# Performance work log

Hardware: AMD Instinct MI355X
Metric: run time of the kernel (lower is better)

Reference implementation:

```python
import jax, jax.numpy as jnp
import numpy as np

DIM = 64
HEADS = 4
EPS_LN = 1e-6
EPS_NORM = 1e-12


def _dwconv(x, w):
    # depthwise 3x3, SAME padding; x: [B,C,H,W], w: [C,1,3,3]
    return jax.lax.conv_general_dilated(
        x, w, window_strides=(1, 1), padding='SAME',
        feature_group_count=x.shape[1],
        dimension_numbers=('NCHW', 'OIHW', 'NCHW'))


def setup_inputs() -> dict:
    key = jax.random.key(0)
    ks = jax.random.split(key, 10)
    s = 0.05
    inp = {
        'x': jax.random.normal(ks[0], (8, DIM, 256, 256), dtype=jnp.float32),
        'ln_w': jnp.ones((DIM,), jnp.float32),
        'ln_b': jnp.zeros((DIM,), jnp.float32),
        'w_q': jax.random.normal(ks[1], (DIM, DIM), jnp.float32) * s,
        'w_k': jax.random.normal(ks[2], (DIM, DIM), jnp.float32) * s,
        'w_v': jax.random.normal(ks[3], (DIM, DIM), jnp.float32) * s,
        'dw_q': jax.random.normal(ks[4], (DIM, 1, 3, 3), jnp.float32) * s,
        'dw_k': jax.random.normal(ks[5], (DIM, 1, 3, 3), jnp.float32) * s,
        'dw_v': jax.random.normal(ks[6], (DIM, 1, 3, 3), jnp.float32) * s,
        'w_proj': jax.random.normal(ks[7], (DIM, DIM, 3, 3), jnp.float32) * s,
        'w_comp': jax.random.normal(ks[8], (DIM // 4, DIM), jnp.float32) * s,
        'temperature': jnp.ones((HEADS, 1, 1), jnp.float32),
    }
    return inp


def reference(x, ln_w, ln_b, w_q, w_k, w_v, dw_q, dw_k, dw_v, w_proj, w_comp, temperature):
    b, c, h, w = x.shape
    heads = temperature.shape[0]
    hd = c // heads  # per-head channels

    # LayerNorm over channel dim (per spatial location), biased variance
    mu = jnp.mean(x, axis=1, keepdims=True)
    var = jnp.mean((x - mu) ** 2, axis=1, keepdims=True)
    xn = (x - mu) / jnp.sqrt(var + EPS_LN)
    xn = xn * ln_w[None, :, None, None] + ln_b[None, :, None, None]

    # 1x1 projections then depthwise 3x3
    q = _dwconv(jnp.einsum('oc,bchw->bohw', w_q, xn), dw_q)
    k = _dwconv(jnp.einsum('oc,bchw->bohw', w_k, xn), dw_k)
    v = _dwconv(jnp.einsum('oc,bchw->bohw', w_v, xn), dw_v)

    # [b, heads, hd, h*w]
    q = q.reshape(b, heads, hd, h * w)
    k = k.reshape(b, heads, hd, h * w)
    v = v.reshape(b, heads, hd, h * w)

    # L2 normalize along spatial axis (torch F.normalize: x / max(||x||, eps))
    q = q / jnp.maximum(jnp.linalg.norm(q, axis=-1, keepdims=True), EPS_NORM)
    k = k / jnp.maximum(jnp.linalg.norm(k, axis=-1, keepdims=True), EPS_NORM)

    # channel attention: [b, heads, hd, hd]
    attn = jnp.einsum('bhcn,bhdn->bhcd', q, k) * temperature[None]
    attn = jax.nn.softmax(attn, axis=-1)
    out = jnp.einsum('bhcd,bhdn->bhcn', attn, v).reshape(b, c, h, w)

    # 3x3 projection + residual (residual is the normalized x, per source)
    out = jax.lax.conv_general_dilated(
        out, w_proj, window_strides=(1, 1), padding='SAME',
        dimension_numbers=('NCHW', 'OIHW', 'NCHW')) + xn

    # 1x1 compress to dim//4
    return jnp.einsum('oc,bchw->bohw', w_comp, out)
```

## Files before the change

### kernel.cpp

```cpp
#include <hip/hip_runtime.h>
#include <hip/hip_bf16.h>
#include <stdint.h>

#define BB 8
#define CC 64
#define HH 256
#define WW 256
#define NPIX 65536
#define HEADS 4
#define HD 16
#define PRS 76

using bf16 = __hip_bfloat16;
typedef __attribute__((ext_vector_type(8))) short short8;
typedef __attribute__((ext_vector_type(4))) float f32x4;

__device__ __forceinline__ float bf2f(bf16 v) { return __bfloat162float(v); }
__device__ __forceinline__ bf16 f2bf(float v) { return __float2bfloat16(v); }
__device__ __forceinline__ short f2bfs(float f) { bf16 h = __float2bfloat16(f); return *reinterpret_cast<short*>(&h); }
__device__ __forceinline__ float bfs2f(short s) { return __uint_as_float(((uint32_t)(uint16_t)s) << 16); }
__device__ __forceinline__ uint32_t pk2(float a, float b) {
  return (uint32_t)(uint16_t)f2bfs(a) | ((uint32_t)(uint16_t)f2bfs(b) << 16);
}
__device__ __forceinline__ short8 zero8() { short8 z = {0, 0, 0, 0, 0, 0, 0, 0}; return z; }

__global__ void k_prep(const float* __restrict__ w_comp, const float* __restrict__ w_proj,
                       const float* __restrict__ w_q, const float* __restrict__ w_k,
                       const float* __restrict__ w_v,
                       short* __restrict__ wcpb, short* __restrict__ wqkvb,
                       short* __restrict__ wcb) {
  int idx = blockIdx.x * 256 + threadIdx.x;
  if (idx < 9 * 16 * 64) {
    int c = idx & 63;
    int o = (idx >> 6) & 15;
    int kk = idx >> 10;
    float acc = 0.f;
    for (int m = 0; m < 64; ++m)
      acc += w_comp[o * 64 + m] * w_proj[(m * 64 + c) * 9 + kk];
    wcpb[idx] = f2bfs(acc);
  }
  if (idx < 3 * 4096) {
    const float* Ws[3] = {w_q, w_k, w_v};
    wqkvb[idx] = f2bfs(Ws[idx >> 12][idx & 4095]);
  }
  if (idx < 1024) wcb[idx] = f2bfs(w_comp[idx]);
}

__global__ __launch_bounds__(256)
void k_ln(const float* __restrict__ x, const float* __restrict__ ln_w,
          const float* __restrict__ ln_b, short* __restrict__ xnb) {
  const int tid = threadIdx.x;
  const int b = blockIdx.x >> 8;
  const int n = ((blockIdx.x & 255) << 8) + tid;
  const float* xp = x + (size_t)b * CC * NPIX + n;
  float v[64];
  float s = 0.f, s2 = 0.f;
#pragma unroll
  for (int c = 0; c < 64; ++c) {
    float t0 = xp[(size_t)c * NPIX];
    v[c] = t0; s += t0; s2 += t0 * t0;
  }
  const float mu = s * (1.f / 64.f);
  const float r = rsqrtf(s2 * (1.f / 64.f) - mu * mu + 1e-6f);
  short* op = xnb + ((size_t)b * NPIX + n) * 64;
#pragma unroll
  for (int c8 = 0; c8 < 8; ++c8) {
    uint32_t pk[4];
#pragma unroll
    for (int j = 0; j < 4; ++j) {
      const int c0 = c8 * 8 + 2 * j;
      float f0 = (v[c0] - mu) * r * ln_w[c0] + ln_b[c0];
      float f1 = (v[c0 + 1] - mu) * r * ln_w[c0 + 1] + ln_b[c0 + 1];
      pk[j] = pk2(f0, f1);
    }
    *reinterpret_cast<uint4*>(op + c8 * 8) = make_uint4(pk[0], pk[1], pk[2], pk[3]);
  }
}

__global__ __launch_bounds__(512)
void k_qkv(const short* __restrict__ xnb, const short* __restrict__ wqkvb,
           const short* __restrict__ wcb,
           const float* __restrict__ dw_q, const float* __restrict__ dw_k,
           const float* __restrict__ dw_v,
           bf16* __restrict__ qo, bf16* __restrict__ ko,
           short* __restrict__ aov, short* __restrict__ res16) {
  __shared__ short pr_s[336 * PRS];
  const int tid = threadIdx.x;
  const int lane = tid & 63;
  const int wv = tid >> 6;
  const int olocal = lane & 15;
  const int g = lane >> 4;
  const int t = blockIdx.y;
  const int tx = blockIdx.x & 15, ty = (blockIdx.x >> 4) & 15, b = blockIdx.x >> 8;
  const int x0 = tx * 16 - 1, y0 = ty * 16 - 1;

  if (t == 0) {
    short8 wc0 = *reinterpret_cast<const short8*>(wcb + olocal * 64 + g * 8);
    short8 wc1 = *reinterpret_cast<const short8*>(wcb + olocal * 64 + 32 + g * 8);
#pragma unroll
    for (int t2 = 0; t2 < 2; ++t2) {
      const int oy = wv * 2 + t2;
      const int n = (ty * 16 + oy) * WW + tx * 16 + olocal;
      const short* bb = xnb + ((size_t)b * NPIX + n) * 64 + g * 8;
      short8 b0 = *reinterpret_cast<const short8*>(bb);
      short8 b1 = *reinterpret_cast<const short8*>(bb + 32);
      f32x4 acc = {0.f, 0.f, 0.f, 0.f};
      acc = __builtin_amdgcn_mfma_f32_16x16x32_bf16(wc0, b0, acc, 0, 0, 0);
      acc = __builtin_amdgcn_mfma_f32_16x16x32_bf16(wc1, b1, acc, 0, 0, 0);
      uint2 st;
      st.x = pk2(acc[0], acc[1]);
      st.y = pk2(acc[2], acc[3]);
      *reinterpret_cast<uint2*>(&res16[((size_t)b * NPIX + n) * 16 + g * 4]) = st;
    }
  }

  short8 Bt[4][2];
#pragma unroll
  for (int ot = 0; ot < 4; ++ot) {
    const short* wb = wqkvb + t * 4096 + (ot * 16 + olocal) * 64 + g * 8;
    Bt[ot][0] = *reinterpret_cast<const short8*>(wb);
    Bt[ot][1] = *reinterpret_cast<const short8*>(wb + 32);
  }

  short8 a0[3], a1[3];
#pragma unroll
  for (int j = 0; j < 3; ++j) {
    const int pt = wv + j * 8;
    const int p = pt * 16 + olocal;
    const int py = y0 + p / 18;
    const int px_ = x0 + p % 18;
    const bool vld = (pt < 21) && (p < 324) && ((unsigned)py < 256u) && ((unsigned)px_ < 256u);
    if (vld) {
      const short* ab = xnb + ((size_t)b * NPIX + py * WW + px_) * 64 + g * 8;
      a0[j] = *reinterpret_cast<const short8*>(ab);
      a1[j] = *reinterpret_cast<const short8*>(ab + 32);
    } else {
      a0[j] = zero8();
      a1[j] = zero8();
    }
  }
#pragma unroll
  for (int j = 0; j < 3; ++j) {
    const int pt = wv + j * 8;
    if (pt >= 21) continue;
    const int p2 = pt * 16 + olocal;
#pragma unroll
    for (int ot = 0; ot < 4; ++ot) {
      f32x4 acc = {0.f, 0.f, 0.f, 0.f};
      acc = __builtin_amdgcn_mfma_f32_16x16x32_bf16(Bt[ot][0], a0[j], acc, 0, 0, 0);
      acc = __builtin_amdgcn_mfma_f32_16x16x32_bf16(Bt[ot][1], a1[j], acc, 0, 0, 0);
      uint2 st;
      st.x = pk2(acc[0], acc[1]);
      st.y = pk2(acc[2], acc[3]);
      *reinterpret_cast<uint2*>(&pr_s[p2 * PRS + ot * 16 + g * 4]) = st;
    }
  }
  __syncthreads();

  const float* dmt = (t == 0) ? dw_q : (t == 1) ? dw_k : dw_v;
  float dmr[8][9];
#pragma unroll
  for (int u = 0; u < 8; ++u)
#pragma unroll
    for (int kk = 0; kk < 9; ++kk)
      dmr[u][kk] = dmt[(wv * 8 + u) * 9 + kk];
  bf16* ob = ((t == 0) ? qo : ko) + (size_t)b * CC * NPIX;
#pragma unroll
  for (int i = 0; i < 4; ++i) {
    const int pxl = lane + i * 64;
    const int oy = pxl >> 4, ox = pxl & 15;
    float acc8[8] = {0.f, 0.f, 0.f, 0.f, 0.f, 0.f, 0.f, 0.f};
#pragma unroll
    for (int ky = 0; ky < 3; ++ky)
#pragma unroll
      for (int kx = 0; kx < 3; ++kx) {
        const short8 pv = *reinterpret_cast<const short8*>(
            &pr_s[((oy + ky) * 18 + ox + kx) * PRS + wv * 8]);
        const int kk = ky * 3 + kx;
#pragma unroll
        for (int u = 0; u < 8; ++u)
          acc8[u] += dmr[u][kk] * bfs2f(pv[u]);
      }
    const int n = (ty * 16 + oy) * WW + tx * 16 + ox;
    if (t < 2) {
#pragma unroll
      for (int u = 0; u < 8; ++u)
        ob[(size_t)(wv * 8 + u) * NPIX + n] = f2bf(acc8[u]);
    } else {
      uint4 st = make_uint4(pk2(acc8[0], acc8[1]), pk2(acc8[2], acc8[3]),
                            pk2(acc8[4], acc8[5]), pk2(acc8[6], acc8[7]));
      *reinterpret_cast<uint4*>(&aov[((size_t)b * NPIX + n) * 64 + wv * 8]) = st;
    }
  }
}

__global__ __launch_bounds__(256)
void k_logits(const bf16* __restrict__ q, const bf16* __restrict__ kk_,
              float* __restrict__ Spart, float* __restrict__ Qpart,
              float* __restrict__ Kpart) {
  const int tid = threadIdx.x;
  const int lane = tid & 63;
  const int wv = tid >> 6;
  const int bh = blockIdx.x >> 5;
  const int chunk = blockIdx.x & 31;
  const int row = lane & 15;
  const int g = lane >> 4;
  const short* qp = (const short*)q + (size_t)(bh * HD + row) * NPIX;
  const short* kp = (const short*)kk_ + (size_t)(bh * HD + row) * NPIX;
  const int n0 = chunk * 2048 + wv * 512 + g * 8;
  f32x4 s = {0.f, 0.f, 0.f, 0.f};
  f32x4 sq = {0.f, 0.f, 0.f, 0.f};
  f32x4 sk = {0.f, 0.f, 0.f, 0.f};
#pragma unroll
  for (int it = 0; it < 16; ++it) {
    const int n = n0 + it * 32;
    short8 qa = *reinterpret_cast<const short8*>(qp + n);
    short8 ka = *reinterpret_cast<const short8*>(kp + n);
    s  = __builtin_amdgcn_mfma_f32_16x16x32_bf16(qa, ka, s, 0, 0, 0);
    sq = __builtin_amdgcn_mfma_f32_16x16x32_bf16(qa, qa, sq, 0, 0, 0);
    sk = __builtin_amdgcn_mfma_f32_16x16x32_bf16(ka, ka, sk, 0, 0, 0);
  }
  const size_t tile = (size_t)blockIdx.x * 4 + wv;
  float* sp = Spart + tile * 256;
#pragma unroll
  for (int r = 0; r < 4; ++r)
    sp[(g * 4 + r) * 16 + row] = s[r];
  if ((row >> 2) == g) {
    Qpart[tile * 16 + row] = sq[row & 3];
    Kpart[tile * 16 + row] = sk[row & 3];
  }
}

__global__ __launch_bounds__(256)
void k_softmax(const float* __restrict__ Spart, const float* __restrict__ Qpart,
               const float* __restrict__ Kpart, const float* __restrict__ temp,
               short* __restrict__ attb) {
  const int tid = threadIdx.x;
  const int bh = blockIdx.x;
  const int b = bh >> 2, h = bh & 3;
  const int i = tid >> 4, j = tid & 15;
  float S = 0.f, qs = 0.f, ks = 0.f;
  const size_t t0 = (size_t)bh * 128;
  for (int c = 0; c < 128; ++c) {
    S += Spart[(t0 + c) * 256 + tid];
    qs += Qpart[(t0 + c) * 16 + i];
    ks += Kpart[(t0 + c) * 16 + j];
  }
  float nq = fmaxf(sqrtf(qs), 1e-12f);
  float nk = fmaxf(sqrtf(ks), 1e-12f);
  float val = S / (nq * nk) * temp[h];
  float m = val;
  for (int d = 1; d < 16; d <<= 1) m = fmaxf(m, __shfl_xor(m, d));
  float e = __expf(val - m);
  float s = e;
  for (int d = 1; d < 16; d <<= 1) s += __shfl_xor(s, d);
  attb[((size_t)b * 64 + h * 16 + i) * 64 + h * 16 + j] = f2bfs(e / s);
#pragma unroll
  for (int mq = 0; mq < 4; ++mq) {
    const int idx = tid * 4 + mq;
    const int r = idx >> 6, c = idx & 63;
    if ((c >> 4) != h)
      attb[((size_t)b * 64 + h * 16 + r) * 64 + c] = 0;
  }
}

__global__ __launch_bounds__(512)
void k_attf(const short* __restrict__ attb, const short* __restrict__ vao,
            const short* __restrict__ wcpb, const short* __restrict__ res16,
            float* __restrict__ out) {
  __shared__ short ao_s[336 * PRS];
  const int tid = threadIdx.x;
  const int lane = tid & 63;
  const int wv = tid >> 6;
  const int olocal = lane & 15;
  const int g = lane >> 4;
  const int tx = blockIdx.x & 15, ty = (blockIdx.x >> 4) & 15, b = blockIdx.x >> 8;
  const int x0 = tx * 16 - 1, y0 = ty * 16 - 1;

  {
    short8 AT[4][2];
#pragma unroll
    for (int ot = 0; ot < 4; ++ot) {
      const short* ab = attb + ((size_t)b * 64 + ot * 16 + olocal) * 64 + g * 8;
      AT[ot][0] = *reinterpret_cast<const short8*>(ab);
      AT[ot][1] = *reinterpret_cast<const short8*>(ab + 32);
    }
#pragma unroll
    for (int j = 0; j < 3; ++j) {
      const int pt = wv + j * 8;
      if (pt >= 21) continue;
      const int p = pt * 16 + olocal;
      const int py = y0 + p / 18;
      const int px_ = x0 + p % 18;
      const bool vld = (p < 324) && ((unsigned)py < 256u) && ((unsigned)px_ < 256u);
      short8 b0 = zero8(), b1 = zero8();
      if (vld) {
        const short* vp = vao + ((size_t)b * NPIX + py * WW + px_) * 64 + g * 8;
        b0 = *reinterpret_cast<const short8*>(vp);
        b1 = *reinterpret_cast<const short8*>(vp + 32);
      }
#pragma unroll
      for (int ot = 0; ot < 4; ++ot) {
        f32x4 acc = {0.f, 0.f, 0.f, 0.f};
        acc = __builtin_amdgcn_mfma_f32_16x16x32_bf16(AT[ot][0], b0, acc, 0, 0, 0);
        acc = __builtin_amdgcn_mfma_f32_16x16x32_bf16(AT[ot][1], b1, acc, 0, 0, 0);
        uint2 st;
        st.x = pk2(acc[0], acc[1]);
        st.y = pk2(acc[2], acc[3]);
        *reinterpret_cast<uint2*>(&ao_s[p * PRS + ot * 16 + g * 4]) = st;
      }
    }
  }
  __syncthreads();

  short8 WA[9][2];
#pragma unroll
  for (int kk = 0; kk < 9; ++kk) {
    const short* wb = wcpb + (kk * 16 + olocal) * 64 + g * 8;
    WA[kk][0] = *reinterpret_cast<const short8*>(wb);
    WA[kk][1] = *reinterpret_cast<const short8*>(wb + 32);
  }
#pragma unroll
  for (int s = 0; s < 2; ++s) {
    const int oy = wv * 2 + s;
    const int n0 = (ty * 16 + oy) * WW + tx * 16;
    uint2 rv = *reinterpret_cast<const uint2*>(
        &res16[((size_t)b * NPIX + n0 + olocal) * 16 + g * 4]);
    f32x4 acc;
    acc[0] = __uint_as_float(rv.x << 16);
    acc[1] = __uint_as_float(rv.x & 0xffff0000u);
    acc[2] = __uint_as_float(rv.y << 16);
    acc[3] = __uint_as_float(rv.y & 0xffff0000u);
#pragma unroll
    for (int ky = 0; ky < 3; ++ky)
#pragma unroll
      for (int kx = 0; kx < 3; ++kx) {
        const int hp = (oy + ky) * 18 + olocal + kx;
        short8 b0 = *reinterpret_cast<const short8*>(&ao_s[hp * PRS + g * 8]);
        short8 b1 = *reinterpret_cast<const short8*>(&ao_s[hp * PRS + 32 + g * 8]);
        acc = __builtin_amdgcn_mfma_f32_16x16x32_bf16(WA[ky * 3 + kx][0], b0, acc, 0, 0, 0);
        acc = __builtin_amdgcn_mfma_f32_16x16x32_bf16(WA[ky * 3 + kx][1], b1, acc, 0, 0, 0);
      }
    float* op = out + ((size_t)b * 16 + g * 4) * NPIX + n0 + olocal;
    op[0] = acc[0];
    op[NPIX] = acc[1];
    op[2 * NPIX] = acc[2];
    op[3 * NPIX] = acc[3];
  }
}

extern "C" void kernel_launch(void* const* d_in, const int* in_sizes, int n_in,
                              void* d_out, int out_size, void* d_ws, size_t ws_size,
                              hipStream_t stream) {
  const float* x      = (const float*)d_in[0];
  const float* ln_w   = (const float*)d_in[1];
  const float* ln_b   = (const float*)d_in[2];
  const float* w_q    = (const float*)d_in[3];
  const float* w_k    = (const float*)d_in[4];
  const float* w_v    = (const float*)d_in[5];
  const float* dw_q   = (const float*)d_in[6];
  const float* dw_k   = (const float*)d_in[7];
  const float* dw_v   = (const float*)d_in[8];
  const float* w_proj = (const float*)d_in[9];
  const float* w_comp = (const float*)d_in[10];
  const float* temp   = (const float*)d_in[11];
  float* out = (float*)d_out;

  const size_t SPX = (size_t)BB * NPIX;
  short* xnb   = (short*)d_ws;
  short* qb    = xnb + SPX * 64;
  short* kb    = qb + SPX * 64;
  short* aov   = kb + SPX * 64;
  short* res16 = aov + SPX * 64;
  short* wcpb  = res16 + SPX * 16;
  short* wqkvb = wcpb + 9216;
  short* wcb   = wqkvb + 12288;
  short* attb  = wcb + 1024;
  float* Spart = (float*)(attb + 8 * 64 * 64 + 512);
  float* Qpart = Spart + 4096 * 256;
  float* Kpart = Qpart + 4096 * 16;

  k_prep<<<52, 256, 0, stream>>>(w_comp, w_proj, w_q, w_k, w_v, wcpb, wqkvb, wcb);
  k_ln<<<2048, 256, 0, stream>>>(x, ln_w, ln_b, xnb);
  dim3 gqkv(2048, 3);
  k_qkv<<<gqkv, 512, 0, stream>>>(xnb, wqkvb, wcb, dw_q, dw_k, dw_v,
                                  (bf16*)qb, (bf16*)kb, aov, res16);
  k_logits<<<1024, 256, 0, stream>>>((const bf16*)qb, (const bf16*)kb, Spart, Qpart, Kpart);
  k_softmax<<<32, 256, 0, stream>>>(Spart, Qpart, Kpart, temp, attb);
  k_attf<<<2048, 512, 0, stream>>>(attb, aov, wcpb, res16, out);
}
```

Before: 313.3 us.

## Process two tiles per qkv block with double-buffered LDS overlapping loads and dwconv

Each k_qkv block now handles two adjacent 16x16 spatial tiles, which halves the grid. The shared projection buffer is double-buffered so the global loads for the second tile are issued before the first tile's depthwise conv runs. The depthwise conv also switches to packed float2 arithmetic on bf16 pairs, unpacked from uint32 words. The intent is to hide global load latency and amortize per-block weight loads, at the cost of doubled LDS per block (about 98KB), which may lower occupancy.

```diff
diff --git a/kernel.cpp b/kernel.cpp
--- a/kernel.cpp
+++ b/kernel.cpp
@@ -14,6 +14,7 @@
 using bf16 = __hip_bfloat16;
 typedef __attribute__((ext_vector_type(8))) short short8;
 typedef __attribute__((ext_vector_type(4))) float f32x4;
+typedef __attribute__((ext_vector_type(2))) float f32x2;
 
 __device__ __forceinline__ float bf2f(bf16 v) { return __bfloat162float(v); }
 __device__ __forceinline__ bf16 f2bf(float v) { return __float2bfloat16(v); }
@@ -23,6 +24,12 @@
   return (uint32_t)(uint16_t)f2bfs(a) | ((uint32_t)(uint16_t)f2bfs(b) << 16);
 }
 __device__ __forceinline__ short8 zero8() { short8 z = {0, 0, 0, 0, 0, 0, 0, 0}; return z; }
+__device__ __forceinline__ f32x2 unpk2(uint32_t w) {
+  f32x2 r;
+  r.x = __uint_as_float(w << 16);
+  r.y = __uint_as_float(w & 0xffff0000u);
+  return r;
+}
 
 __global__ void k_prep(const float* __restrict__ w_comp, const float* __restrict__ w_proj,
                        const float* __restrict__ w_q, const float* __restrict__ w_k,
@@ -84,33 +91,37 @@
            const float* __restrict__ dw_v,
            bf16* __restrict__ qo, bf16* __restrict__ ko,
            short* __restrict__ aov, short* __restrict__ res16) {
-  __shared__ short pr_s[336 * PRS];
+  __shared__ short pr2[2][324 * PRS];
   const int tid = threadIdx.x;
   const int lane = tid & 63;
   const int wv = tid >> 6;
   const int olocal = lane & 15;
   const int g = lane >> 4;
   const int t = blockIdx.y;
-  const int tx = blockIdx.x & 15, ty = (blockIdx.x >> 4) & 15, b = blockIdx.x >> 8;
-  const int x0 = tx * 16 - 1, y0 = ty * 16 - 1;
+  const int tx0 = (blockIdx.x & 7) * 2;
+  const int ty = (blockIdx.x >> 3) & 15;
+  const int b = blockIdx.x >> 7;
 
   if (t == 0) {
     short8 wc0 = *reinterpret_cast<const short8*>(wcb + olocal * 64 + g * 8);
     short8 wc1 = *reinterpret_cast<const short8*>(wcb + olocal * 64 + 32 + g * 8);
 #pragma unroll
-    for (int t2 = 0; t2 < 2; ++t2) {
-      const int oy = wv * 2 + t2;
-      const int n = (ty * 16 + oy) * WW + tx * 16 + olocal;
-      const short* bb = xnb + ((size_t)b * NPIX + n) * 64 + g * 8;
-      short8 b0 = *reinterpret_cast<const short8*>(bb);
-      short8 b1 = *reinterpret_cast<const short8*>(bb + 32);
-      f32x4 acc = {0.f, 0.f, 0.f, 0.f};
-      acc = __builtin_amdgcn_mfma_f32_16x16x32_bf16(wc0, b0, acc, 0, 0, 0);
-      acc = __builtin_amdgcn_mfma_f32_16x16x32_bf16(wc1, b1, acc, 0, 0, 0);
-      uint2 st;
-      st.x = pk2(acc[0], acc[1]);
-      st.y = pk2(acc[2], acc[3]);
-      *reinterpret_cast<uint2*>(&res16[((size_t)b * NPIX + n) * 16 + g * 4]) = st;
+    for (int tile = 0; tile < 2; ++tile) {
+#pragma unroll
+      for (int t2 = 0; t2 < 2; ++t2) {
+        const int oy = wv * 2 + t2;
+        const int n = (ty * 16 + oy) * WW + (tx0 + tile) * 16 + olocal;
+        const short* bb = xnb + ((size_t)b * NPIX + n) * 64 + g * 8;
+        short8 b0 = *reinterpret_cast<const short8*>(bb);
+        short8 b1 = *reinterpret_cast<const short8*>(bb + 32);
+        f32x4 acc = {0.f, 0.f, 0.f, 0.f};
+        acc = __builtin_amdgcn_mfma_f32_16x16x32_bf16(wc0, b0, acc, 0, 0, 0);
+        acc = __builtin_amdgcn_mfma_f32_16x16x32_bf16(wc1, b1, acc, 0, 0, 0);
+        uint2 st;
+        st.x = pk2(acc[0], acc[1]);
+        st.y = pk2(acc[2], acc[3]);
+        *reinterpret_cast<uint2*>(&res16[((size_t)b * NPIX + n) * 16 + g * 4]) = st;
+      }
     }
   }
 
@@ -122,76 +133,110 @@
     Bt[ot][1] = *reinterpret_cast<const short8*>(wb + 32);
   }
 
+  const float* dmt = (t == 0) ? dw_q : (t == 1) ? dw_k : dw_v;
+  bf16* ob = ((t == 0) ? qo : ko) + (size_t)b * CC * NPIX;
+
   short8 a0[3], a1[3];
-#pragma unroll
-  for (int j = 0; j < 3; ++j) {
-    const int pt = wv + j * 8;
-    const int p = pt * 16 + olocal;
-    const int py = y0 + p / 18;
-    const int px_ = x0 + p % 18;
-    const bool vld = (pt < 21) && (p < 324) && ((unsigned)py < 256u) && ((unsigned)px_ < 256u);
-    if (vld) {
-      const short* ab = xnb + ((size_t)b * NPIX + py * WW + px_) * 64 + g * 8;
-      a0[j] = *reinterpret_cast<const short8*>(ab);
-      a1[j] = *reinterpret_cast<const short8*>(ab + 32);
-    } else {
-      a0[j] = zero8();
-      a1[j] = zero8();
-    }
-  }
-#pragma unroll
-  for (int j = 0; j < 3; ++j) {
-    const int pt = wv + j * 8;
-    if (pt >= 21) continue;
-    const int p2 = pt * 16 + olocal;
-#pragma unroll
-    for (int ot = 0; ot < 4; ++ot) {
-      f32x4 acc = {0.f, 0.f, 0.f, 0.f};
-      acc = __builtin_amdgcn_mfma_f32_16x16x32_bf16(Bt[ot][0], a0[j], acc, 0, 0, 0);
-      acc = __builtin_amdgcn_mfma_f32_16x16x32_bf16(Bt[ot][1], a1[j], acc, 0, 0, 0);
-      uint2 st;
-      st.x = pk2(acc[0], acc[1]);
-      st.y = pk2(acc[2], acc[3]);
-      *reinterpret_cast<uint2*>(&pr_s[p2 * PRS + ot * 16 + g * 4]) = st;
-    }
-  }
+
+#define PH2_LOADS(txc)                                                              \
+  {                                                                                 \
+    const int x0 = (txc) * 16 - 1, y0 = ty * 16 - 1;                                \
+    _Pragma("unroll")                                                               \
+    for (int j = 0; j < 3; ++j) {                                                   \
+      const int pt = wv + j * 8;                                                    \
+      const int p = pt * 16 + olocal;                                               \
+      const int py = y0 + p / 18;                                                   \
+      const int px_ = x0 + p % 18;                                                  \
+      const bool vld = (pt < 21) && (p < 324) &&                                    \
+                       ((unsigned)py < 256u) && ((unsigned)px_ < 256u);             \
+      if (vld) {                                                                    \
+        const short* ab = xnb + ((size_t)b * NPIX + py * WW + px_) * 64 + g * 8;    \
+        a0[j] = *reinterpret_cast<const short8*>(ab);                               \
+        a1[j] = *reinterpret_cast<const short8*>(ab + 32);                          \
+      } else {                                                                      \
+        a0[j] = zero8();                                                            \
+        a1[j] = zero8();                                                            \
+      }                                                                             \
+    }                                                                               \
+  }
+
+#define PH2_MFMA(buf)                                                               \
+  {                                                                                 \
+    _Pragma("unroll")                                                               \
+    for (int j = 0; j < 3; ++j) {                                                   \
+      const int pt = wv + j * 8;                                                    \
+      if (pt >= 21) continue;                                                       \
+      const int p2 = pt * 16 + olocal;                                              \
+      _Pragma("unroll")                                                             \
+      for (int ot = 0; ot < 4; ++ot) {                                              \
+        f32x4 acc = {0.f, 0.f, 0.f, 0.f};                                           \
+        acc = __builtin_amdgcn_mfma_f32_16x16x32_bf16(Bt[ot][0], a0[j], acc, 0, 0, 0); \
+        acc = __builtin_amdgcn_mfma_f32_16x16x32_bf16(Bt[ot][1], a1[j], acc, 0, 0, 0); \
+        uint2 st;                                                                   \
+        st.x = pk2(acc[0], acc[1]);                                                 \
+        st.y = pk2(acc[2], acc[3]);                                                 \
+        *reinterpret_cast<uint2*>(&(buf)[p2 * PRS + ot * 16 + g * 4]) = st;         \
+      }                                                                             \
+    }                                                                               \
+  }
+
+#define PH3(buf, txc)                                                               \
+  {                                                                                 \
+    f32x2 dm2[9][4];                                                                \
+    _Pragma("unroll")                                                               \
+    for (int u2 = 0; u2 < 4; ++u2)                                                  \
+      _Pragma("unroll")                                                             \
+      for (int kk = 0; kk < 9; ++kk) {                                              \
+        dm2[kk][u2].x = dmt[(wv * 8 + 2 * u2) * 9 + kk];                            \
+        dm2[kk][u2].y = dmt[(wv * 8 + 2 * u2 + 1) * 9 + kk];                        \
+      }                                                                             \
+    _Pragma("unroll")                                                               \
+    for (int i = 0; i < 4; ++i) {                                                   \
+      const int pxl = lane + i * 64;                                                \
+      const int oy = pxl >> 4, ox = pxl & 15;                                       \
+      f32x2 ac0 = {0.f, 0.f}, ac1 = {0.f, 0.f}, ac2 = {0.f, 0.f}, ac3 = {0.f, 0.f}; \
+      _Pragma("unroll")                                                             \
+      for (int ky = 0; ky < 3; ++ky)                                                \
+        _Pragma("unroll")                                                           \
+        for (int kx = 0; kx < 3; ++kx) {                                            \
+          const uint4 pw = *reinterpret_cast<const uint4*>(                         \
+              &(buf)[((oy + ky) * 18 + ox + kx) * PRS + wv * 8]);                   \
+          const int kk = ky * 3 + kx;                                               \
+          ac0 += dm2[kk][0] * unpk2(pw.x);                                          \
+          ac1 += dm2[kk][1] * unpk2(pw.y);                                          \
+          ac2 += dm2[kk][2] * unpk2(pw.z);                                          \
+          ac3 += dm2[kk][3] * unpk2(pw.w);                                          \
+        }                                                                           \
+      const int n = (ty * 16 + oy) * WW + (txc) * 16 + ox;                          \
+      if (t < 2) {                                                                  \
+        ob[(size_t)(wv * 8 + 0) * NPIX + n] = f2bf(ac0.x);                          \
+        ob[(size_t)(wv * 8 + 1) * NPIX + n] = f2bf(ac0.y);                          \
+        ob[(size_t)(wv * 8 + 2) * NPIX + n] = f2bf(ac1.x);                          \
+        ob[(size_t)(wv * 8 + 3) * NPIX + n] = f2bf(ac1.y);                          \
+        ob[(size_t)(wv * 8 + 4) * NPIX + n] = f2bf(ac2.x);                          \
+        ob[(size_t)(wv * 8 + 5) * NPIX + n] = f2bf(ac2.y);                          \
+        ob[(size_t)(wv * 8 + 6) * NPIX + n] = f2bf(ac3.x);                          \
+        ob[(size_t)(wv * 8 + 7) * NPIX + n] = f2bf(ac3.y);                          \
+      } else {                                                                      \
+        uint4 st = make_uint4(pk2(ac0.x, ac0.y), pk2(ac1.x, ac1.y),                 \
+                              pk2(ac2.x, ac2.y), pk2(ac3.x, ac3.y));                \
+        *reinterpret_cast<uint4*>(&aov[((size_t)b * NPIX + n) * 64 + wv * 8]) = st; \
+      }                                                                             \
+    }                                                                               \
+  }
+
+  PH2_LOADS(tx0);
+  PH2_MFMA(pr2[0]);
   __syncthreads();
-
-  const float* dmt = (t == 0) ? dw_q : (t == 1) ? dw_k : dw_v;
-  float dmr[8][9];
-#pragma unroll
-  for (int u = 0; u < 8; ++u)
-#pragma unroll
-    for (int kk = 0; kk < 9; ++kk)
-      dmr[u][kk] = dmt[(wv * 8 + u) * 9 + kk];
-  bf16* ob = ((t == 0) ? qo : ko) + (size_t)b * CC * NPIX;
-#pragma unroll
-  for (int i = 0; i < 4; ++i) {
-    const int pxl = lane + i * 64;
-    const int oy = pxl >> 4, ox = pxl & 15;
-    float acc8[8] = {0.f, 0.f, 0.f, 0.f, 0.f, 0.f, 0.f, 0.f};
-#pragma unroll
-    for (int ky = 0; ky < 3; ++ky)
-#pragma unroll
-      for (int kx = 0; kx < 3; ++kx) {
-        const short8 pv = *reinterpret_cast<const short8*>(
-            &pr_s[((oy + ky) * 18 + ox + kx) * PRS + wv * 8]);
-        const int kk = ky * 3 + kx;
-#pragma unroll
-        for (int u = 0; u < 8; ++u)
-          acc8[u] += dmr[u][kk] * bfs2f(pv[u]);
-      }
-    const int n = (ty * 16 + oy) * WW + tx * 16 + ox;
-    if (t < 2) {
-#pragma unroll
-      for (int u = 0; u < 8; ++u)
-        ob[(size_t)(wv * 8 + u) * NPIX + n] = f2bf(acc8[u]);
-    } else {
-      uint4 st = make_uint4(pk2(acc8[0], acc8[1]), pk2(acc8[2], acc8[3]),
-                            pk2(acc8[4], acc8[5]), pk2(acc8[6], acc8[7]));
-      *reinterpret_cast<uint4*>(&aov[((size_t)b * NPIX + n) * 64 + wv * 8]) = st;
-    }
-  }
+  PH2_LOADS(tx0 + 1);
+  PH3(pr2[0], tx0);
+  PH2_MFMA(pr2[1]);
+  __syncthreads();
+  PH3(pr2[1], tx0 + 1);
+
+#undef PH2_LOADS
+#undef PH2_MFMA
+#undef PH3
 }
 
 __global__ __launch_bounds__(256)
@@ -382,7 +427,7 @@
 
   k_prep<<<52, 256, 0, stream>>>(w_comp, w_proj, w_q, w_k, w_v, wcpb, wqkvb, wcb);
   k_ln<<<2048, 256, 0, stream>>>(x, ln_w, ln_b, xnb);
-  dim3 gqkv(2048, 3);
+  dim3 gqkv(1024, 3);
   k_qkv<<<gqkv, 512, 0, stream>>>(xnb, wqkvb, wcb, dw_q, dw_k, dw_v,
                                   (bf16*)qb, (bf16*)kb, aov, res16);
   k_logits<<<1024, 256, 0, stream>>>((const bf16*)qb, (const bf16*)kb, Spart, Qpart, Kpart);
```

New measurement: 330.6 us. +5.5%, slower.
